# Kernel optimization log

Measured on AMD Instinct MI355X. Metric: run time of the kernel, lower is better.

The kernel has to match this reference:

```python
import jax, jax.numpy as jnp
import numpy as np

B, C, NQ, NK, S, H, FF = 8, 256, 1024, 4096, 16, 8, 2048
DH = C // H
EPS = 1e-5


def _layernorm(x, g, b):
    m = jnp.mean(x, axis=-1, keepdims=True)
    v = jnp.mean((x - m) ** 2, axis=-1, keepdims=True)
    return (x - m) * jax.lax.rsqrt(v + EPS) * g + b


def _box_query(key_pos, query_pos):
    # key_pos: (B,NK,3); query_pos: (B,NQ,6) = centers ++ box sizes (L,H,W)
    centers = query_pos[:, :, None, :3]            # (B,NQ,1,3)
    half = 0.5 * query_pos[:, :, None, 3:]         # (B,NQ,1,3)
    off = jnp.abs(key_pos[:, None, :, :] - centers)  # (B,NQ,NK,3)
    inside = jnp.all(off <= half, axis=-1)         # (B,NQ,NK)
    # first n_sample inside-points in index order (stable sort: inside first)
    order = jnp.argsort(~inside, axis=-1, stable=True)
    idx = order[..., :S]                           # (B,NQ,S)
    valid = jnp.take_along_axis(inside, idx, axis=-1)
    mask = ~valid                                  # True = padded / masked
    idx = jnp.where(mask, 0, idx)
    mask = mask.at[..., 0].set(False)              # matches cuda path: slot 0 never masked
    return idx, mask


def _forward(query, key, query_pos, key_pos,
             q_w, q_b, k_w, k_b, v_w, v_b, o_w, o_b,
             lin1_w, lin1_b, lin2_w, lin2_b,
             n1_g, n1_b, n2_g, n2_b, qpe_w, qpe_b, kpe_w, kpe_b):
    idx, mask = _box_query(key_pos, query_pos)     # (B,NQ,S), (B,NQ,S)
    # gather neighborhoods
    gxyz = jax.vmap(lambda kp, ix: kp[ix])(key_pos, idx)        # (B,NQ,S,3)
    gxyz = gxyz - query_pos[:, :, None, :3]                     # center-relative
    gfeat = jax.vmap(lambda kf, ix: kf[:, ix])(key, idx)        # (B,C,NQ,S)

    BQ = B * NQ
    kfeat = jnp.transpose(gfeat, (0, 2, 3, 1)).reshape(BQ, S, C)   # (BQ,S,C)
    kpe = gxyz.reshape(BQ, S, 3) @ kpe_w.T + kpe_b                 # cross_embed
    qtok = jnp.transpose(query, (0, 2, 1)).reshape(BQ, C)          # (BQ,C)
    qpe = (query_pos @ qpe_w.T + qpe_b).reshape(BQ, C)             # pos_embed

    # multihead cross-attention: 1 query vs S=16 local keys per group
    kv_in = kfeat + kpe
    qh = ((qtok + qpe) @ q_w.T + q_b).reshape(BQ, H, DH)
    kh = (kv_in @ k_w.T + k_b).reshape(BQ, S, H, DH)
    vh = (kv_in @ v_w.T + v_b).reshape(BQ, S, H, DH)
    scores = jnp.einsum('bhd,bshd->bhs', qh, kh) / np.sqrt(DH)    # (BQ,H,S)
    scores = jnp.where(mask.reshape(BQ, 1, S), -1e30, scores)
    attn = jax.nn.softmax(scores, axis=-1)
    ao = jnp.einsum('bhs,bshd->bhd', attn, vh).reshape(BQ, C)
    ao = ao @ o_w.T + o_b

    x = _layernorm(qtok + ao, n1_g, n1_b)                         # post-norm
    ff = jax.nn.relu(x @ lin1_w.T + lin1_b) @ lin2_w.T + lin2_b
    x = _layernorm(x + ff, n2_g, n2_b)
    return jnp.transpose(x.reshape(B, NQ, C), (0, 2, 1))          # (B,C,NQ)


def setup_inputs() -> dict:
    rng = jax.random.key(0)
    ks = jax.random.split(rng, 24)
    s = 0.02
    query = jax.random.normal(ks[0], (B, C, NQ), jnp.float32)
    key = jax.random.normal(ks[1], (B, C, NK), jnp.float32)
    key_pos = jax.random.uniform(ks[2], (B, NK, 3), jnp.float32)
    centers = jax.random.uniform(ks[3], (B, NQ, 3), jnp.float32)
    sizes = jax.random.uniform(ks[4], (B, NQ, 3), jnp.float32, minval=0.1, maxval=0.4)
    query_pos = jnp.concatenate([centers, sizes], axis=-1)
    p = {
        'q_w': jax.random.normal(ks[5], (C, C)) * s, 'q_b': jnp.zeros((C,)),
        'k_w': jax.random.normal(ks[6], (C, C)) * s, 'k_b': jnp.zeros((C,)),
        'v_w': jax.random.normal(ks[7], (C, C)) * s, 'v_b': jnp.zeros((C,)),
        'o_w': jax.random.normal(ks[8], (C, C)) * s, 'o_b': jnp.zeros((C,)),
        'lin1_w': jax.random.normal(ks[9], (FF, C)) * s, 'lin1_b': jnp.zeros((FF,)),
        'lin2_w': jax.random.normal(ks[10], (C, FF)) * s, 'lin2_b': jnp.zeros((C,)),
        'n1_g': jnp.ones((C,)), 'n1_b': jnp.zeros((C,)),
        'n2_g': jnp.ones((C,)), 'n2_b': jnp.zeros((C,)),
        'qpe_w': jax.random.normal(ks[11], (C, 6)) * s, 'qpe_b': jnp.zeros((C,)),
        'kpe_w': jax.random.normal(ks[12], (C, 3)) * s, 'kpe_b': jnp.zeros((C,)),
    }
    return dict(query=query, key=key, query_pos=query_pos, key_pos=key_pos, **p)


def reference(query, key, query_pos, key_pos,
              q_w, q_b, k_w, k_b, v_w, v_b, o_w, o_b,
              lin1_w, lin1_b, lin2_w, lin2_b,
              n1_g, n1_b, n2_g, n2_b, qpe_w, qpe_b, kpe_w, kpe_b):
    return _forward(query, key, query_pos, key_pos,
                    q_w, q_b, k_w, k_b, v_w, v_b, o_w, o_b,
                    lin1_w, lin1_b, lin2_w, lin2_b,
                    n1_g, n1_b, n2_g, n2_b, qpe_w, qpe_b, kpe_w, kpe_b)
```

## Files before the change

kernel.cpp:

```cpp
#include <hip/hip_runtime.h>
#include <cstdint>

#define B_   8
#define C_   256
#define NQ_  1024
#define NK_  4096
#define S_   16
#define H_   8
#define FF_  2048
#define DH_  32
#define BQ_  (B_*NQ_)
#define EPS_ 1e-5f

typedef __bf16 bf16x8 __attribute__((ext_vector_type(8)));
typedef __bf16 bf16x4 __attribute__((ext_vector_type(4)));
typedef float  f32x4  __attribute__((ext_vector_type(4)));

struct CvtArgs {
  const float* src[6];
  __bf16* dst[6];
};

__device__ __forceinline__ void gload_lds16(const void* g, void* l) {
  __builtin_amdgcn_global_load_lds(
      (const __attribute__((address_space(1))) void*)g,
      (__attribute__((address_space(3))) void*)l, 16, 0, 0);
}

#define SEGA 2048
#define SEGB 10240
#define SEGC 12288
#define SEGD 13568
#define NPREP 13584

__global__ __launch_bounds__(256) void k_prep(
    const float* __restrict__ query, const float* __restrict__ key,
    const float* __restrict__ query_pos, const float* __restrict__ key_pos,
    const float* __restrict__ qpe_w, const float* __restrict__ qpe_b,
    const float* __restrict__ k_w, const float* __restrict__ k_b,
    const float* __restrict__ v_w, const float* __restrict__ v_b,
    const float* __restrict__ kpe_w, const float* __restrict__ kpe_b,
    CvtArgs ca,
    __bf16* __restrict__ keyTb, __bf16* __restrict__ qtokb,
    __bf16* __restrict__ qinb,
    float4* __restrict__ Pk, float4* __restrict__ Pv,
    int* __restrict__ idxo, int* __restrict__ masko) {
  __shared__ __align__(16) float smem[1248];
  int blk = blockIdx.x, t = threadIdx.x;
  int tx = t & 31, ty = t >> 5;

  if (blk < SEGA) {
    int lane = t & 63;
    int q = blk * 4 + (t >> 6);
    int b = q >> 10;
    const float* kpb = key_pos + (size_t)b * NK_ * 3;
    const float* qp = query_pos + (size_t)q * 6;
    float cx = qp[0], cy = qp[1], cz = qp[2];
    float hx = 0.5f * qp[3], hy = 0.5f * qp[4], hz = 0.5f * qp[5];
    int* iq = idxo + (size_t)q * S_;
    int found = 0;
    for (int ch = 0; ch < NK_ / 64; ch += 4) {
      float dx[4], dy[4], dz[4];
#pragma unroll
      for (int u = 0; u < 4; ++u) {
        int k = (ch + u) * 64 + lane;
        dx[u] = fabsf(kpb[k * 3 + 0] - cx);
        dy[u] = fabsf(kpb[k * 3 + 1] - cy);
        dz[u] = fabsf(kpb[k * 3 + 2] - cz);
      }
#pragma unroll
      for (int u = 0; u < 4; ++u) {
        bool inside = (dx[u] <= hx) && (dy[u] <= hy) && (dz[u] <= hz);
        unsigned long long bal = __ballot(inside);
        if (inside) {
          int slot = found + __popcll(bal & ((1ull << lane) - 1ull));
          if (slot < S_) iq[slot] = (ch + u) * 64 + lane;
        }
        found += __popcll(bal);
      }
      if (found >= S_) break;
    }
    if (found > S_) found = S_;
    if (lane < S_) {
      int m = (lane < found) ? 0 : 1;
      if (lane >= found) iq[lane] = 0;
      if (lane == 0) m = 0;
      masko[(size_t)q * S_ + lane] = m;
    }
  } else if (blk < SEGB) {
    int local = blk - SEGA;
    float (*tt)[33] = (float(*)[33])smem;
    int x = local & 127, y = (local >> 7) & 7, z = local >> 10;
    int j0 = x * 32, i0 = y * 32;
    const float* inz = key + (size_t)z * C_ * NK_;
    __bf16* outz = keyTb + (size_t)z * NK_ * C_;
#pragma unroll
    for (int r = 0; r < 32; r += 8)
      tt[ty + r][tx] = inz[(size_t)(i0 + ty + r) * NK_ + (j0 + tx)];
    __syncthreads();
#pragma unroll
    for (int r = 0; r < 32; r += 8)
      outz[(size_t)(j0 + ty + r) * C_ + (i0 + tx)] = (__bf16)tt[tx][ty + r];
  } else if (blk < SEGC) {
    int local = blk - SEGB;
    float (*tt)[33] = (float(*)[33])smem;
    float (*sqp)[6] = (float(*)[6])(smem + 1056);
    int x = local & 31, y = (local >> 5) & 7, z = local >> 8;
    int nq0 = x * 32, c0 = y * 32;
    const float* inz = query + (size_t)z * C_ * NQ_;
#pragma unroll
    for (int r = 0; r < 32; r += 8)
      tt[ty + r][tx] = inz[(size_t)(c0 + ty + r) * NQ_ + (nq0 + tx)];
    if (t < 192)
      sqp[t / 6][t % 6] = query_pos[((size_t)z * NQ_ + nq0 + t / 6) * 6 + (t % 6)];
    int c = c0 + tx;
    float w0 = qpe_w[c * 6 + 0], w1 = qpe_w[c * 6 + 1], w2 = qpe_w[c * 6 + 2];
    float w3 = qpe_w[c * 6 + 3], w4 = qpe_w[c * 6 + 4], w5 = qpe_w[c * 6 + 5];
    float wb = qpe_b[c];
    __syncthreads();
#pragma unroll
    for (int r = 0; r < 32; r += 8) {
      int nql = ty + r;
      size_t row = (size_t)z * NQ_ + nq0 + nql;
      float v = tt[tx][nql];
      float pe = wb + sqp[nql][0] * w0 + sqp[nql][1] * w1 + sqp[nql][2] * w2 +
                 sqp[nql][3] * w3 + sqp[nql][4] * w4 + sqp[nql][5] * w5;
      qtokb[row * C_ + c] = (__bf16)v;
      qinb[row * C_ + c] = (__bf16)(v + pe);
    }
  } else if (blk < SEGD) {
    int local = blk - SEGC;
    int idx, base;
    if (local < 64)       { idx = 0; base = local; }
    else if (local < 128) { idx = 1; base = local - 64; }
    else if (local < 192) { idx = 2; base = local - 128; }
    else if (local < 256) { idx = 3; base = local - 192; }
    else if (local < 768) { idx = 4; base = local - 256; }
    else                  { idx = 5; base = local - 768; }
    size_t off = (size_t)base * 1024 + t * 4;
    float4 v = *(const float4*)(ca.src[idx] + off);
    __bf16* o = ca.dst[idx] + off;
    o[0] = (__bf16)v.x; o[1] = (__bf16)v.y; o[2] = (__bf16)v.z; o[3] = (__bf16)v.w;
  } else {
    int local = blk - SEGD;
    int bx = local & 7, bv = local >> 3;
    const float* w  = bv ? v_w : k_w;
    const float* wb = bv ? v_b : k_b;
    float4* P = bv ? Pv : Pk;
    float4 (*red)[8] = (float4(*)[8])smem;
    int nl = t >> 3, ks = (t & 7) * 32;
    int n = bx * 32 + nl;
    const float* wr = w + (size_t)n * C_;
    float p0 = 0.f, p1 = 0.f, p2 = 0.f, pb = 0.f;
#pragma unroll
    for (int k = ks; k < ks + 32; ++k) {
      float wv = wr[k];
      p0 += kpe_w[k * 3 + 0] * wv;
      p1 += kpe_w[k * 3 + 1] * wv;
      p2 += kpe_w[k * 3 + 2] * wv;
      pb += kpe_b[k] * wv;
    }
    red[nl][t & 7] = make_float4(p0, p1, p2, pb);
    __syncthreads();
    if (t < 32) {
      float4 s = red[t][0];
#pragma unroll
      for (int j = 1; j < 8; ++j) {
        float4 r = red[t][j];
        s.x += r.x; s.y += r.y; s.z += r.z; s.w += r.w;
      }
      s.w += wb[bx * 32 + t];
      P[bx * 32 + t] = s;
    }
  }
}

template <int BM, int BN>
__device__ __forceinline__ void gemm_tile(
    const __bf16* __restrict__ A, const __bf16* __restrict__ Wn,
    int m0, int n0, int K, int kbeg, int kend,
    __bf16 (*As)[64], __bf16 (*Bs)[64],
    f32x4 (&acc)[BM / 32][BN / 32]) {
  constexpr int MI = BM / 32, JN = BN / 32;
  constexpr int AI = BM / 32, BI = BN / 32;
  int t = threadIdx.x;
  int lane = t & 63, w = t >> 6;
  int lane16 = lane & 15, quad = lane >> 4;
  int wm = (w & 1) * (BM / 2), wn = (w >> 1) * (BN / 2);
  int l3 = lane >> 3;
  int lc = lane & 7;

  for (int k0 = kbeg; k0 < kend; k0 += 64) {
#pragma unroll
    for (int i = 0; i < AI; ++i) {
      int j = i * 4 + w;
      int row = j * 8 + l3;
      const __bf16* src = A + (size_t)(m0 + row) * K + k0 + ((lc ^ l3) << 3);
      gload_lds16(src, (char*)&As[0][0] + j * 1024);
    }
#pragma unroll
    for (int i = 0; i < BI; ++i) {
      int j = i * 4 + w;
      int row = j * 8 + l3;
      const __bf16* src = Wn + (size_t)(n0 + row) * K + k0 + ((lc ^ l3) << 3);
      gload_lds16(src, (char*)&Bs[0][0] + j * 1024);
    }
    __syncthreads();
#pragma unroll
    for (int kk = 0; kk < 64; kk += 32) {
      bf16x8 af[MI], bfr[JN];
      int qc = (kk >> 3) + quad;
#pragma unroll
      for (int i = 0; i < MI; ++i) {
        int row = wm + i * 16 + lane16;
        int ch = qc ^ (lane16 & 7);
        af[i] = *(const bf16x8*)((const char*)&As[row][0] + ch * 16);
      }
#pragma unroll
      for (int j = 0; j < JN; ++j) {
        int row = wn + j * 16 + lane16;
        int ch = qc ^ (lane16 & 7);
        bfr[j] = *(const bf16x8*)((const char*)&Bs[row][0] + ch * 16);
      }
#pragma unroll
      for (int i = 0; i < MI; ++i)
#pragma unroll
        for (int j = 0; j < JN; ++j)
          acc[i][j] = __builtin_amdgcn_mfma_f32_16x16x32_bf16(af[i], bfr[j], acc[i][j], 0, 0, 0);
    }
    __syncthreads();
  }
}

template <int BM, int BN, int RELU, int OUT_BF16>
__device__ __forceinline__ void gemm_body(
    const __bf16* __restrict__ A, const __bf16* __restrict__ Wn,
    const float* __restrict__ bias, void* __restrict__ outp,
    int n0, int m0, int N, int K, int kbeg, int kend) {
  constexpr int MI = BM / 32, JN = BN / 32;
  __shared__ __align__(16) __bf16 As[BM][64];
  __shared__ __align__(16) __bf16 Bs[BN][64];
  int t = threadIdx.x;
  int lane = t & 63, w = t >> 6;
  int lane16 = lane & 15, quad = lane >> 4;
  int wm = (w & 1) * (BM / 2), wn = (w >> 1) * (BN / 2);

  f32x4 acc[MI][JN];
#pragma unroll
  for (int i = 0; i < MI; ++i)
#pragma unroll
    for (int j = 0; j < JN; ++j) acc[i][j] = (f32x4){0.f, 0.f, 0.f, 0.f};

  gemm_tile<BM, BN>(A, Wn, m0, n0, K, kbeg, kend, As, Bs, acc);

#pragma unroll
  for (int j = 0; j < JN; ++j) {
    int col = n0 + wn + j * 16 + lane16;
    float bv = bias ? bias[col] : 0.f;
#pragma unroll
    for (int i = 0; i < MI; ++i) {
#pragma unroll
      for (int r = 0; r < 4; ++r) {
        int row = m0 + wm + i * 16 + quad * 4 + r;
        float v = acc[i][j][r] + bv;
        if (RELU) v = fmaxf(v, 0.f);
        if (OUT_BF16)
          ((__bf16*)outp)[(size_t)row * N + col] = (__bf16)v;
        else
          ((float*)outp)[(size_t)row * N + col] = v;
      }
    }
  }
}

template <int BM, int BN, int RELU, int OUT_BF16>
__global__ __launch_bounds__(256) void k_gemm(
    const __bf16* __restrict__ A, const __bf16* __restrict__ Wn,
    const float* __restrict__ bias, void* __restrict__ outp, int N, int K) {
  gemm_body<BM, BN, RELU, OUT_BF16>(A, Wn, bias, outp,
                                    blockIdx.x * BN, blockIdx.y * BM, N, K, 0, K);
}

__global__ __launch_bounds__(256) void k_gemm2(
    const __bf16* __restrict__ keyTb, const __bf16* __restrict__ kvwb,
    __bf16* __restrict__ khvbuf,
    const __bf16* __restrict__ qinb, const __bf16* __restrict__ qwb,
    const float* __restrict__ q_b, __bf16* __restrict__ qhb) {
  int blk = blockIdx.x;
  const __bf16 *A, *Wn; const float* bias; __bf16* outp; int n0, m0, N;
  if (blk < 1024) {
    A = keyTb; Wn = kvwb; bias = nullptr; outp = khvbuf;
    n0 = (blk & 3) * 128; m0 = (blk >> 2) * 128; N = 512;
  } else {
    int l = blk - 1024;
    A = qinb; Wn = qwb; bias = q_b; outp = qhb;
    n0 = (l & 1) * 128; m0 = (l >> 1) * 128; N = 256;
  }
  gemm_body<128, 128, 0, 1>(A, Wn, bias, outp, n0, m0, N, 256, 0, 256);
}

template <int K>
__device__ __forceinline__ void gemm32x256_sk2(
    const __bf16* __restrict__ A, const __bf16* __restrict__ Wn,
    const float* __restrict__ bias, int m0, char* smem, float (*buf)[257]) {
  constexpr int NT = K / 2 / 64;
  int t = threadIdx.x;
  int lane = t & 63, w = t >> 6;
  int kg = w >> 2, wl = w & 3;
  int lane16 = lane & 15, quad = lane >> 4;
  int wm = (wl & 1) * 16, wn = (wl >> 1) * 128;
  int l3 = lane >> 3, lc = lane & 7;
  int kbase = kg * (K / 2);

  char* As0 = smem + kg * 8192;
  char* Bs0 = smem + 16384 + kg * 65536;

  f32x4 acc[8];
#pragma unroll
  for (int j = 0; j < 8; ++j) acc[j] = (f32x4){0.f, 0.f, 0.f, 0.f};

  auto STAGE = [&](int bi, int ts) {
    int k0 = kbase + ts * 64;
    {
      int j = wl;
      int row = j * 8 + l3;
      const __bf16* src = A + (size_t)(m0 + row) * K + k0 + ((lc ^ l3) << 3);
      gload_lds16(src, As0 + bi * 4096 + j * 1024);
    }
#pragma unroll
    for (int i = 0; i < 8; ++i) {
      int j = i * 4 + wl;
      int row = j * 8 + l3;
      const __bf16* src = Wn + (size_t)row * K + k0 + ((lc ^ l3) << 3);
      gload_lds16(src, Bs0 + bi * 32768 + j * 1024);
    }
  };

  STAGE(0, 0);
  __syncthreads();
  int cur = 0;
  for (int ts = 0; ts < NT; ++ts) {
    if (ts + 1 < NT) STAGE(cur ^ 1, ts + 1);
    const char* Ab = As0 + cur * 4096;
    const char* Bb = Bs0 + cur * 32768;
#pragma unroll
    for (int kk = 0; kk < 64; kk += 32) {
      int qc = (kk >> 3) + quad;
      int ch = qc ^ (lane16 & 7);
      bf16x8 af = *(const bf16x8*)(Ab + (wm + lane16) * 128 + ch * 16);
      bf16x8 bfr[8];
#pragma unroll
      for (int j = 0; j < 8; ++j)
        bfr[j] = *(const bf16x8*)(Bb + (wn + j * 16 + lane16) * 128 + ch * 16);
#pragma unroll
      for (int j = 0; j < 8; ++j)
        acc[j] = __builtin_amdgcn_mfma_f32_16x16x32_bf16(af, bfr[j], acc[j], 0, 0, 0);
    }
    __syncthreads();
    cur ^= 1;
  }

  if (kg == 1) {
#pragma unroll
    for (int j = 0; j < 8; ++j) {
      int col = wn + j * 16 + lane16;
#pragma unroll
      for (int r = 0; r < 4; ++r)
        buf[wm + quad * 4 + r][col] = acc[j][r];
    }
  }
  __syncthreads();
  if (kg == 0) {
#pragma unroll
    for (int j = 0; j < 8; ++j) {
      int col = wn + j * 16 + lane16;
      float bv = bias[col];
#pragma unroll
      for (int r = 0; r < 4; ++r) {
        int row = wm + quad * 4 + r;
        buf[row][col] += acc[j][r] + bv;
      }
    }
  }
  __syncthreads();
}

__global__ __launch_bounds__(512) void k_oln(
    const __bf16* __restrict__ A , const __bf16* __restrict__ Wn ,
    const float* __restrict__ obias, const __bf16* __restrict__ qtokb,
    const float* __restrict__ g, const float* __restrict__ bb,
    __bf16* __restrict__ x1b) {
  __shared__ __align__(16) char smem[147456];
  float (*buf)[257] = (float(*)[257])smem;
  int m0 = blockIdx.x * 32;
  gemm32x256_sk2<C_>(A, Wn, obias, m0, smem, buf);

  int t = threadIdx.x;
  int lane = t & 63, w = t >> 6;
  float4 g4 = *(const float4*)(g + lane * 4);
  float4 b4 = *(const float4*)(bb + lane * 4);
#pragma unroll
  for (int rr = 0; rr < 4; ++rr) {
    int row = w * 4 + rr;
    size_t grow = (size_t)(m0 + row);
    bf16x4 q4 = *(const bf16x4*)&qtokb[grow * C_ + lane * 4];
    float x0 = buf[row][lane * 4 + 0] + (float)q4[0];
    float x1 = buf[row][lane * 4 + 1] + (float)q4[1];
    float x2 = buf[row][lane * 4 + 2] + (float)q4[2];
    float x3 = buf[row][lane * 4 + 3] + (float)q4[3];
    float s = x0 + x1 + x2 + x3;
#pragma unroll
    for (int off = 32; off >= 1; off >>= 1) s += __shfl_xor(s, off);
    float mean = s * (1.f / C_);
    float d0 = x0 - mean, d1 = x1 - mean, d2 = x2 - mean, d3 = x3 - mean;
    float v = d0 * d0 + d1 * d1 + d2 * d2 + d3 * d3;
#pragma unroll
    for (int off = 32; off >= 1; off >>= 1) v += __shfl_xor(v, off);
    float inv = 1.f / sqrtf(v * (1.f / C_) + EPS_);
    __bf16* obp = x1b + grow * C_ + lane * 4;
    obp[0] = (__bf16)(d0 * inv * g4.x + b4.x);
    obp[1] = (__bf16)(d1 * inv * g4.y + b4.y);
    obp[2] = (__bf16)(d2 * inv * g4.z + b4.z);
    obp[3] = (__bf16)(d3 * inv * g4.w + b4.w);
  }
}

__global__ __launch_bounds__(512) void k_ff2lnt(
    const __bf16* __restrict__ A , const __bf16* __restrict__ Wn ,
    const float* __restrict__ l2bias, const __bf16* __restrict__ x1b,
    const float* __restrict__ g, const float* __restrict__ bb,
    float* __restrict__ out) {
  __shared__ __align__(16) char smem[147456];
  float (*buf)[257] = (float(*)[257])smem;
  int m0 = blockIdx.x * 32;
  gemm32x256_sk2<FF_>(A, Wn, l2bias, m0, smem, buf);

  int t = threadIdx.x;
  int lane = t & 63, w = t >> 6;
  float4 g4 = *(const float4*)(g + lane * 4);
  float4 b4 = *(const float4*)(bb + lane * 4);
#pragma unroll
  for (int rr = 0; rr < 4; ++rr) {
    int row = w * 4 + rr;
    size_t grow = (size_t)(m0 + row);
    bf16x4 v4 = *(const bf16x4*)&x1b[grow * C_ + lane * 4];
    float x0 = buf[row][lane * 4 + 0] + (float)v4[0];
    float x1 = buf[row][lane * 4 + 1] + (float)v4[1];
    float x2 = buf[row][lane * 4 + 2] + (float)v4[2];
    float x3 = buf[row][lane * 4 + 3] + (float)v4[3];
    float s = x0 + x1 + x2 + x3;
#pragma unroll
    for (int off = 32; off >= 1; off >>= 1) s += __shfl_xor(s, off);
    float mean = s * (1.f / C_);
    float d0 = x0 - mean, d1 = x1 - mean, d2 = x2 - mean, d3 = x3 - mean;
    float v = d0 * d0 + d1 * d1 + d2 * d2 + d3 * d3;
#pragma unroll
    for (int off = 32; off >= 1; off >>= 1) v += __shfl_xor(v, off);
    float inv = 1.f / sqrtf(v * (1.f / C_) + EPS_);
    buf[row][lane * 4 + 0] = d0 * inv * g4.x + b4.x;
    buf[row][lane * 4 + 1] = d1 * inv * g4.y + b4.y;
    buf[row][lane * 4 + 2] = d2 * inv * g4.z + b4.z;
    buf[row][lane * 4 + 3] = d3 * inv * g4.w + b4.w;
  }
  __syncthreads();
  int z = m0 >> 10, nq0 = m0 & (NQ_ - 1);
  int tx = t & 31, ty = t >> 5;
#pragma unroll
  for (int ci = 0; ci < 16; ++ci) {
    int c = ci * 16 + ty;
    out[((size_t)z * C_ + c) * NQ_ + nq0 + tx] = buf[tx][c];
  }
}

__global__ __launch_bounds__(256) void k_attnf(
    const __bf16* __restrict__ khv,
    const float* __restrict__ key_pos,
    const float* __restrict__ query_pos,
    const int* __restrict__ idx,
    const int* __restrict__ maskb,
    const __bf16* __restrict__ qhb,
    const float4* __restrict__ Pk,
    const float4* __restrict__ Pv,
    __bf16* __restrict__ aob) {
  __shared__ __bf16 kvs[S_][520];
  __shared__ float qrow[C_];
  __shared__ float sc[H_][S_];
  __shared__ float pw[H_][S_];
  __shared__ float4 gx4[S_];
  __shared__ float4 pgxs[H_];
  __shared__ float4 qpks[H_];
  __shared__ int srow[S_], smask[S_];
  int bq = blockIdx.x, b = bq >> 10, t = threadIdx.x;

  if (t < S_) {
    int k = idx[(size_t)bq * S_ + t];
    srow[t] = b * NK_ + k;
    smask[t] = maskb[(size_t)bq * S_ + t];
    const float* kpp = key_pos + ((size_t)b * NK_ + k) * 3;
    const float* qp  = query_pos + (size_t)bq * 6;
    gx4[t] = make_float4(kpp[0] - qp[0], kpp[1] - qp[1], kpp[2] - qp[2], 1.f);
  }
  float qv_t = (float)qhb[(size_t)bq * C_ + t];
  qrow[t] = qv_t;
  {
    float4 p = Pk[t];
    p.x *= qv_t; p.y *= qv_t; p.z *= qv_t; p.w *= qv_t;
#pragma unroll
    for (int off = 16; off >= 1; off >>= 1) {
      p.x += __shfl_xor(p.x, off);
      p.y += __shfl_xor(p.y, off);
      p.z += __shfl_xor(p.z, off);
      p.w += __shfl_xor(p.w, off);
    }
    if ((t & 31) == 0) {
      const float s = 0.17677669529663687f;
      qpks[t >> 5] = make_float4(p.x * s, p.y * s, p.z * s, p.w * s);
    }
  }
  __syncthreads();
  {
    int s = t >> 4, c0 = (t & 15) * 32;
    const __bf16* src = khv + (size_t)srow[s] * 512 + c0;
    *(bf16x8*)&kvs[s][c0]      = *(const bf16x8*)&src[0];
    *(bf16x8*)&kvs[s][c0 + 8]  = *(const bf16x8*)&src[8];
    *(bf16x8*)&kvs[s][c0 + 16] = *(const bf16x8*)&src[16];
    *(bf16x8*)&kvs[s][c0 + 24] = *(const bf16x8*)&src[24];
  }
  __syncthreads();
  if (t < H_ * S_) {
    int h = t >> 4, s = t & (S_ - 1);
    float d = 0.f;
#pragma unroll
    for (int c0 = 0; c0 < 32; c0 += 8) {
      bf16x8 xv = *(const bf16x8*)&kvs[s][h * 32 + c0];
#pragma unroll
      for (int j = 0; j < 8; ++j) d += qrow[h * 32 + c0 + j] * (float)xv[j];
    }
    d *= 0.17677669529663687f;
    float4 g = gx4[s];
    float4 pk = qpks[h];
    d += g.x * pk.x + g.y * pk.y + g.z * pk.z + pk.w;
    if (smask[s]) d = -1e30f;
    sc[h][s] = d;
  }
  __syncthreads();
  if (t < H_) {
    float mx = -3.4e38f;
#pragma unroll
    for (int s = 0; s < S_; ++s) mx = fmaxf(mx, sc[t][s]);
    float e[S_], sum = 0.f;
#pragma unroll
    for (int s = 0; s < S_; ++s) { e[s] = expf(sc[t][s] - mx); sum += e[s]; }
    float inv = 1.f / sum;
    float gxx = 0.f, gyy = 0.f, gzz = 0.f;
#pragma unroll
    for (int s = 0; s < S_; ++s) {
      float p = e[s] * inv;
      pw[t][s] = p;
      float4 g = gx4[s];
      gxx += p * g.x; gyy += p * g.y; gzz += p * g.z;
    }
    pgxs[t] = make_float4(gxx, gyy, gzz, 1.f);
  }
  __syncthreads();
  {
    int h = t >> 5;
    float a = 0.f;
#pragma unroll
    for (int s = 0; s < S_; ++s) a += pw[h][s] * (float)kvs[s][256 + t];
    float4 pv = Pv[t];
    float4 g = pgxs[h];
    a += g.x * pv.x + g.y * pv.y + g.z * pv.z + pv.w;
    aob[(size_t)bq * C_ + t] = (__bf16)a;
  }
}

extern "C" void kernel_launch(void* const* d_in, const int* in_sizes, int n_in,
                              void* d_out, int out_size, void* d_ws, size_t ws_size,
                              hipStream_t stream) {
  const float* query     = (const float*)d_in[0];
  const float* key       = (const float*)d_in[1];
  const float* query_pos = (const float*)d_in[2];
  const float* key_pos   = (const float*)d_in[3];
  const float* q_w = (const float*)d_in[4];  const float* q_b = (const float*)d_in[5];
  const float* k_w = (const float*)d_in[6];  const float* k_b = (const float*)d_in[7];
  const float* v_w = (const float*)d_in[8];  const float* v_b = (const float*)d_in[9];
  const float* o_w = (const float*)d_in[10]; const float* o_b = (const float*)d_in[11];
  const float* lin1_w = (const float*)d_in[12]; const float* lin1_b = (const float*)d_in[13];
  const float* lin2_w = (const float*)d_in[14]; const float* lin2_b = (const float*)d_in[15];
  const float* n1_g = (const float*)d_in[16]; const float* n1_b = (const float*)d_in[17];
  const float* n2_g = (const float*)d_in[18]; const float* n2_b = (const float*)d_in[19];
  const float* qpe_w = (const float*)d_in[20]; const float* qpe_b = (const float*)d_in[21];
  const float* kpe_w = (const float*)d_in[22]; const float* kpe_b = (const float*)d_in[23];
  float* out = (float*)d_out;

  const size_t BQc = (size_t)BQ_ * C_;
  float* w = (float*)d_ws;
  size_t o = 0;
  __bf16* keyTb = (__bf16*)(w + o); o += (size_t)B_ * NK_ * C_ / 2;
  __bf16* qtokb = (__bf16*)(w + o); o += BQc / 2;
  __bf16* khvbuf = (__bf16*)(w + o); o += (size_t)B_ * NK_ * 512 / 2;
  __bf16* qinb = (__bf16*)(w + o); o += BQc / 2;
  __bf16* qhb  = (__bf16*)(w + o); o += BQc / 2;
  __bf16* aob  = (__bf16*)(w + o); o += BQc / 2;
  __bf16* x1b  = (__bf16*)(w + o); o += BQc / 2;
  __bf16* qwb  = (__bf16*)(w + o); o += (size_t)C_ * C_ / 2;
  __bf16* kvwb = (__bf16*)(w + o); o += (size_t)C_ * C_;
  __bf16* owb  = (__bf16*)(w + o); o += (size_t)C_ * C_ / 2;
  __bf16* l1b  = (__bf16*)(w + o); o += (size_t)C_ * FF_ / 2;
  __bf16* l2b  = (__bf16*)(w + o); o += (size_t)C_ * FF_ / 2;
  float4* Pk   = (float4*)(w + o); o += C_ * 4;
  float4* Pv   = (float4*)(w + o); o += C_ * 4;
  int* idxb  = (int*)(w + o); o += (size_t)BQ_ * S_;
  int* maskb = (int*)(w + o); o += (size_t)BQ_ * S_;
  __bf16* ff1b = khvbuf;

  CvtArgs ca;
  ca.src[0] = q_w; ca.dst[0] = qwb;
  ca.src[1] = k_w; ca.dst[1] = kvwb;
  ca.src[2] = v_w; ca.dst[2] = kvwb + (size_t)C_ * C_;
  ca.src[3] = o_w; ca.dst[3] = owb;
  ca.src[4] = lin1_w; ca.dst[4] = l1b;
  ca.src[5] = lin2_w; ca.dst[5] = l2b;
  k_prep<<<NPREP, 256, 0, stream>>>(query, key, query_pos, key_pos,
                                    qpe_w, qpe_b, k_w, k_b, v_w, v_b,
                                    kpe_w, kpe_b, ca,
                                    keyTb, qtokb, qinb, Pk, Pv, idxb, maskb);
  k_gemm2<<<1024 + 128, 256, 0, stream>>>(keyTb, kvwb, khvbuf, qinb, qwb, q_b, qhb);
  k_attnf<<<BQ_, 256, 0, stream>>>(khvbuf, key_pos, query_pos, idxb, maskb,
                                   qhb, Pk, Pv, aob);
  k_oln<<<BQ_ / 32, 512, 0, stream>>>(aob, owb, o_b, qtokb, n1_g, n1_b, x1b);
  k_gemm<128, 128, 1, 1><<<dim3(FF_ / 128, BQ_ / 128), 256, 0, stream>>>(
      x1b, l1b, lin1_b, ff1b, FF_, C_);
  k_ff2lnt<<<BQ_ / 32, 512, 0, stream>>>(ff1b, l2b, lin2_b, x1b, n2_g, n2_b, out);
}
```

Baseline: 246.7 us.

## Fuse FFN lin1 and lin2 into one kernel keeping hidden activations in LDS

Replaces the separate lin1 GEMM (writing a BQ×FF bf16 intermediate to global memory) and the lin2+LayerNorm kernel with one fused k_ffn kernel. Each 32-row block computes 256-wide chunks of the ReLU hidden activation into LDS and immediately multiplies them by the matching lin2 weight slice, streaming W1/W2 tiles through a 3-stage async LDS ring. This removes the 32 MB round trip of the FF intermediate and one launch. In exchange, each block re-reads all of W1 and W2 (L2 traffic), runs with only 256 blocks, and has a long serial dependency chain per block.

```diff
diff --git a/kernel.cpp b/kernel.cpp
--- a/kernel.cpp
+++ b/kernel.cpp
@@ -273,14 +273,6 @@
   }
 }
 
-template <int BM, int BN, int RELU, int OUT_BF16>
-__global__ __launch_bounds__(256) void k_gemm(
-    const __bf16* __restrict__ A, const __bf16* __restrict__ Wn,
-    const float* __restrict__ bias, void* __restrict__ outp, int N, int K) {
-  gemm_body<BM, BN, RELU, OUT_BF16>(A, Wn, bias, outp,
-                                    blockIdx.x * BN, blockIdx.y * BM, N, K, 0, K);
-}
-
 __global__ __launch_bounds__(256) void k_gemm2(
     const __bf16* __restrict__ keyTb, const __bf16* __restrict__ kvwb,
     __bf16* __restrict__ khvbuf,
@@ -425,18 +417,142 @@
   }
 }
 
-__global__ __launch_bounds__(512) void k_ff2lnt(
-    const __bf16* __restrict__ A , const __bf16* __restrict__ Wn ,
-    const float* __restrict__ l2bias, const __bf16* __restrict__ x1b,
+__global__ __launch_bounds__(512) void k_ffn(
+    const __bf16* __restrict__ x1b, const __bf16* __restrict__ W1,
+    const float* __restrict__ b1, const __bf16* __restrict__ W2,
+    const float* __restrict__ b2,
     const float* __restrict__ g, const float* __restrict__ bb,
     float* __restrict__ out) {
-  __shared__ __align__(16) char smem[147456];
+  __shared__ __align__(16) char smem[139264];
   float (*buf)[257] = (float(*)[257])smem;
+  char* Xs   = smem;
+  char* Ps   = smem + 16384;
+  char* ring = smem + 32768;
+  char* b1s  = smem + 131072;
   int m0 = blockIdx.x * 32;
-  gemm32x256_sk2<FF_>(A, Wn, l2bias, m0, smem, buf);
-
   int t = threadIdx.x;
   int lane = t & 63, w = t >> 6;
+  int lane16 = lane & 15, quad = lane >> 4;
+  int l3 = lane >> 3, lc = lane & 7;
+  int cw = w * 32;
+
+  f32x4 acc_out[2][2], acc_p[2][2];
+#pragma unroll
+  for (int i = 0; i < 2; ++i)
+#pragma unroll
+    for (int j = 0; j < 2; ++j) acc_out[i][j] = (f32x4){0.f, 0.f, 0.f, 0.f};
+
+#pragma unroll
+  for (int i = 0; i < 2; ++i) {
+    int j = i * 8 + w;
+    int row = j * 2 + (lane >> 5);
+    const __bf16* src = x1b + (size_t)(m0 + row) * C_ + (((lane & 31) ^ (row & 7)) << 3);
+    gload_lds16(src, Xs + j * 1024);
+  }
+  gload_lds16(b1 + w * 256 + lane * 4, b1s + w * 1024);
+
+  auto ISSUE = [&](int tau) {
+    int fc = tau >> 3, ph = (tau >> 2) & 1, ks = tau & 3;
+    char* dst = ring + (tau % 3) * 32768;
+#pragma unroll
+    for (int i = 0; i < 4; ++i) {
+      int j = i * 8 + w;
+      int row = j * 8 + l3;
+      const __bf16* src;
+      if (ph == 0)
+        src = W1 + (size_t)(fc * 256 + row) * C_ + ks * 64 + ((lc ^ l3) << 3);
+      else
+        src = W2 + (size_t)row * FF_ + fc * 256 + ks * 64 + ((lc ^ l3) << 3);
+      gload_lds16(src, dst + j * 1024);
+    }
+  };
+
+  ISSUE(0);
+  ISSUE(1);
+
+  for (int s = 0; s < 64; ++s) {
+    if (s < 62) {
+      ISSUE(s + 2);
+      asm volatile("s_waitcnt vmcnt(8)" ::: "memory");
+    } else if (s == 62) {
+      asm volatile("s_waitcnt vmcnt(4)" ::: "memory");
+    } else {
+      asm volatile("s_waitcnt vmcnt(0)" ::: "memory");
+    }
+    __builtin_amdgcn_s_barrier();
+    __builtin_amdgcn_sched_barrier(0);
+
+    int fc = s >> 3, ph = (s >> 2) & 1, ks = s & 3;
+    const char* Tb = ring + (s % 3) * 32768;
+    const char* Ab = ph ? Ps : Xs;
+    int qcb = ks * 8;
+
+    if (ph == 0 && ks == 0) {
+#pragma unroll
+      for (int i = 0; i < 2; ++i)
+#pragma unroll
+        for (int j = 0; j < 2; ++j) acc_p[i][j] = (f32x4){0.f, 0.f, 0.f, 0.f};
+    }
+
+#pragma unroll
+    for (int kk = 0; kk < 64; kk += 32) {
+      int q3 = (kk >> 3) + quad;
+      int swz3 = q3 ^ (lane16 & 7);
+      bf16x8 af[2], bfr[2];
+#pragma unroll
+      for (int rt = 0; rt < 2; ++rt)
+        af[rt] = *(const bf16x8*)(Ab + (rt * 16 + lane16) * 512 + (qcb + swz3) * 16);
+#pragma unroll
+      for (int ct = 0; ct < 2; ++ct)
+        bfr[ct] = *(const bf16x8*)(Tb + (cw + ct * 16 + lane16) * 128 + swz3 * 16);
+      if (ph == 0) {
+#pragma unroll
+        for (int rt = 0; rt < 2; ++rt)
+#pragma unroll
+          for (int ct = 0; ct < 2; ++ct)
+            acc_p[rt][ct] = __builtin_amdgcn_mfma_f32_16x16x32_bf16(af[rt], bfr[ct], acc_p[rt][ct], 0, 0, 0);
+      } else {
+#pragma unroll
+        for (int rt = 0; rt < 2; ++rt)
+#pragma unroll
+          for (int ct = 0; ct < 2; ++ct)
+            acc_out[rt][ct] = __builtin_amdgcn_mfma_f32_16x16x32_bf16(af[rt], bfr[ct], acc_out[rt][ct], 0, 0, 0);
+      }
+    }
+
+    if (ph == 0 && ks == 3) {
+#pragma unroll
+      for (int ct = 0; ct < 2; ++ct) {
+        int pcol = cw + ct * 16 + lane16;
+        float b1v = *(const float*)(b1s + (fc * 256 + pcol) * 4);
+#pragma unroll
+        for (int rt = 0; rt < 2; ++rt)
+#pragma unroll
+          for (int r = 0; r < 4; ++r) {
+            int prow = rt * 16 + quad * 4 + r;
+            float v = fmaxf(acc_p[rt][ct][r] + b1v, 0.f);
+            int chunk = pcol >> 3;
+            int byte = prow * 512 + ((chunk ^ (prow & 7)) << 4) + (pcol & 7) * 2;
+            *(__bf16*)(Ps + byte) = (__bf16)v;
+          }
+      }
+      asm volatile("s_waitcnt lgkmcnt(0)" ::: "memory");
+    }
+  }
+  __syncthreads();
+
+#pragma unroll
+  for (int ct = 0; ct < 2; ++ct) {
+    int col = cw + ct * 16 + lane16;
+    float b2v = b2[col];
+#pragma unroll
+    for (int rt = 0; rt < 2; ++rt)
+#pragma unroll
+      for (int r = 0; r < 4; ++r)
+        buf[rt * 16 + quad * 4 + r][col] = acc_out[rt][ct][r] + b2v;
+  }
+  __syncthreads();
+
   float4 g4 = *(const float4*)(g + lane * 4);
   float4 b4 = *(const float4*)(bb + lane * 4);
 #pragma unroll
@@ -463,6 +579,7 @@
     buf[row][lane * 4 + 3] = d3 * inv * g4.w + b4.w;
   }
   __syncthreads();
+
   int z = m0 >> 10, nq0 = m0 & (NQ_ - 1);
   int tx = t & 31, ty = t >> 5;
 #pragma unroll
@@ -613,7 +730,6 @@
   float4* Pv   = (float4*)(w + o); o += C_ * 4;
   int* idxb  = (int*)(w + o); o += (size_t)BQ_ * S_;
   int* maskb = (int*)(w + o); o += (size_t)BQ_ * S_;
-  __bf16* ff1b = khvbuf;
 
   CvtArgs ca;
   ca.src[0] = q_w; ca.dst[0] = qwb;
@@ -630,7 +746,6 @@
   k_attnf<<<BQ_, 256, 0, stream>>>(khvbuf, key_pos, query_pos, idxb, maskb,
                                    qhb, Pk, Pv, aob);
   k_oln<<<BQ_ / 32, 512, 0, stream>>>(aob, owb, o_b, qtokb, n1_g, n1_b, x1b);
-  k_gemm<128, 128, 1, 1><<<dim3(FF_ / 128, BQ_ / 128), 256, 0, stream>>>(
-      x1b, l1b, lin1_b, ff1b, FF_, C_);
-  k_ff2lnt<<<BQ_ / 32, 512, 0, stream>>>(ff1b, l2b, lin2_b, x1b, n2_g, n2_b, out);
-}
+  k_ffn<<<BQ_ / 32, 512, 0, stream>>>(x1b, l1b, lin1_b, l2b, lin2_b,
+                                      n2_g, n2_b, out);
+}
```

New measurement: 254.2 us. +3.0%, slower.

## Use full-width 64-row GEMM tiles for K/V projection and read K directly in attention

Applied to the files above, without the earlier changes.

The fused K/V and Q projection kernel now uses 64-row tiles spanning the full output width (512 or 256 columns), so each A tile is loaded once instead of being reloaded per 128-column block. This roughly halves the K/V block count and uses a large LDS B buffer with more accumulators per thread, which may cut occupancy. In the attention kernel only V rows are staged in shared memory, while K dot products read global memory directly. That removes a barrier and halves the LDS footprint, at the cost of uncoalesced global reads for K.

```diff
diff --git a/kernel.cpp b/kernel.cpp
--- a/kernel.cpp
+++ b/kernel.cpp
@@ -286,17 +286,55 @@
     __bf16* __restrict__ khvbuf,
     const __bf16* __restrict__ qinb, const __bf16* __restrict__ qwb,
     const float* __restrict__ q_b, __bf16* __restrict__ qhb) {
+  __shared__ __align__(16) __bf16 As[64][64];
+  __shared__ __align__(16) __bf16 Bs[512][64];
   int blk = blockIdx.x;
-  const __bf16 *A, *Wn; const float* bias; __bf16* outp; int n0, m0, N;
-  if (blk < 1024) {
-    A = keyTb; Wn = kvwb; bias = nullptr; outp = khvbuf;
-    n0 = (blk & 3) * 128; m0 = (blk >> 2) * 128; N = 512;
+  int t = threadIdx.x;
+  int lane = t & 63, w = t >> 6;
+  int lane16 = lane & 15, quad = lane >> 4;
+
+  if (blk < 512) {
+    int m0 = blk * 64;
+    int wm = (w & 1) * 32, wn = (w >> 1) * 256;
+    f32x4 acc[2][16];
+#pragma unroll
+    for (int i = 0; i < 2; ++i)
+#pragma unroll
+      for (int j = 0; j < 16; ++j) acc[i][j] = (f32x4){0.f, 0.f, 0.f, 0.f};
+    gemm_tile<64, 512>(keyTb, kvwb, m0, 0, 256, 0, 256, As, Bs, acc);
+#pragma unroll
+    for (int j = 0; j < 16; ++j) {
+      int col = wn + j * 16 + lane16;
+#pragma unroll
+      for (int i = 0; i < 2; ++i)
+#pragma unroll
+        for (int r = 0; r < 4; ++r) {
+          int row = m0 + wm + i * 16 + quad * 4 + r;
+          khvbuf[(size_t)row * 512 + col] = (__bf16)acc[i][j][r];
+        }
+    }
   } else {
-    int l = blk - 1024;
-    A = qinb; Wn = qwb; bias = q_b; outp = qhb;
-    n0 = (l & 1) * 128; m0 = (l >> 1) * 128; N = 256;
-  }
-  gemm_body<128, 128, 0, 1>(A, Wn, bias, outp, n0, m0, N, 256, 0, 256);
+    int m0 = (blk - 512) * 64;
+    int wm = (w & 1) * 32, wn = (w >> 1) * 128;
+    f32x4 acc[2][8];
+#pragma unroll
+    for (int i = 0; i < 2; ++i)
+#pragma unroll
+      for (int j = 0; j < 8; ++j) acc[i][j] = (f32x4){0.f, 0.f, 0.f, 0.f};
+    gemm_tile<64, 256>(qinb, qwb, m0, 0, 256, 0, 256, As, Bs, acc);
+#pragma unroll
+    for (int j = 0; j < 8; ++j) {
+      int col = wn + j * 16 + lane16;
+      float bv = q_b[col];
+#pragma unroll
+      for (int i = 0; i < 2; ++i)
+#pragma unroll
+        for (int r = 0; r < 4; ++r) {
+          int row = m0 + wm + i * 16 + quad * 4 + r;
+          qhb[(size_t)row * 256 + col] = (__bf16)(acc[i][j][r] + bv);
+        }
+    }
+  }
 }
 
 template <int K>
@@ -482,7 +520,7 @@
     const float4* __restrict__ Pk,
     const float4* __restrict__ Pv,
     __bf16* __restrict__ aob) {
-  __shared__ __bf16 kvs[S_][520];
+  __shared__ __bf16 vs[S_][264];
   __shared__ float qrow[C_];
   __shared__ float sc[H_][S_];
   __shared__ float pw[H_][S_];
@@ -519,20 +557,18 @@
   }
   __syncthreads();
   {
-    int s = t >> 4, c0 = (t & 15) * 32;
-    const __bf16* src = khv + (size_t)srow[s] * 512 + c0;
-    *(bf16x8*)&kvs[s][c0]      = *(const bf16x8*)&src[0];
-    *(bf16x8*)&kvs[s][c0 + 8]  = *(const bf16x8*)&src[8];
-    *(bf16x8*)&kvs[s][c0 + 16] = *(const bf16x8*)&src[16];
-    *(bf16x8*)&kvs[s][c0 + 24] = *(const bf16x8*)&src[24];
-  }
-  __syncthreads();
+    int s = t >> 4, c0 = (t & 15) * 16;
+    const __bf16* src = khv + (size_t)srow[s] * 512 + 256 + c0;
+    *(bf16x8*)&vs[s][c0]     = *(const bf16x8*)&src[0];
+    *(bf16x8*)&vs[s][c0 + 8] = *(const bf16x8*)&src[8];
+  }
   if (t < H_ * S_) {
     int h = t >> 4, s = t & (S_ - 1);
+    const __bf16* kp = khv + (size_t)srow[s] * 512 + h * 32;
     float d = 0.f;
 #pragma unroll
     for (int c0 = 0; c0 < 32; c0 += 8) {
-      bf16x8 xv = *(const bf16x8*)&kvs[s][h * 32 + c0];
+      bf16x8 xv = *(const bf16x8*)&kp[c0];
 #pragma unroll
       for (int j = 0; j < 8; ++j) d += qrow[h * 32 + c0 + j] * (float)xv[j];
     }
@@ -567,7 +603,7 @@
     int h = t >> 5;
     float a = 0.f;
 #pragma unroll
-    for (int s = 0; s < S_; ++s) a += pw[h][s] * (float)kvs[s][256 + t];
+    for (int s = 0; s < S_; ++s) a += pw[h][s] * (float)vs[s][t];
     float4 pv = Pv[t];
     float4 g = pgxs[h];
     a += g.x * pv.x + g.y * pv.y + g.z * pv.z + pv.w;
@@ -626,7 +662,7 @@
                                     qpe_w, qpe_b, k_w, k_b, v_w, v_b,
                                     kpe_w, kpe_b, ca,
                                     keyTb, qtokb, qinb, Pk, Pv, idxb, maskb);
-  k_gemm2<<<1024 + 128, 256, 0, stream>>>(keyTb, kvwb, khvbuf, qinb, qwb, q_b, qhb);
+  k_gemm2<<<512 + 128, 256, 0, stream>>>(keyTb, kvwb, khvbuf, qinb, qwb, q_b, qhb);
   k_attnf<<<BQ_, 256, 0, stream>>>(khvbuf, key_pos, query_pos, idxb, maskb,
                                    qhb, Pk, Pv, aob);
   k_oln<<<BQ_ / 32, 512, 0, stream>>>(aob, owb, o_b, qtokb, n1_g, n1_b, x1b);
```

New measurement: 253.2 us. +2.6%, slower.

## Replace split-K 32x256 GEMM with 8-warp N-split tiling and halved LDS

Applied to the files above, without the earlier changes.

The shared 32x256 GEMM used by the out-projection+LayerNorm and FF2+LayerNorm kernels drops its two-way split-K. All eight waves now cover the full K range, each owning a 32x32 output slice, and the split-K reduction pass through LDS is removed. Shared memory per block falls from 144KB to 72KB, which could let two blocks share a CU. The cost is a K loop twice as long per block and smaller per-wave tiles, so each wave re-reads the same A fragments.

```diff
diff --git a/kernel.cpp b/kernel.cpp
--- a/kernel.cpp
+++ b/kernel.cpp
@@ -300,39 +300,38 @@
 }
 
 template <int K>
-__device__ __forceinline__ void gemm32x256_sk2(
+__device__ __forceinline__ void gemm32x256_v3(
     const __bf16* __restrict__ A, const __bf16* __restrict__ Wn,
     const float* __restrict__ bias, int m0, char* smem, float (*buf)[257]) {
-  constexpr int NT = K / 2 / 64;
+  constexpr int NT = K / 64;
   int t = threadIdx.x;
   int lane = t & 63, w = t >> 6;
-  int kg = w >> 2, wl = w & 3;
   int lane16 = lane & 15, quad = lane >> 4;
-  int wm = (wl & 1) * 16, wn = (wl >> 1) * 128;
+  int wn = w * 32;
   int l3 = lane >> 3, lc = lane & 7;
-  int kbase = kg * (K / 2);
-
-  char* As0 = smem + kg * 8192;
-  char* Bs0 = smem + 16384 + kg * 65536;
-
-  f32x4 acc[8];
-#pragma unroll
-  for (int j = 0; j < 8; ++j) acc[j] = (f32x4){0.f, 0.f, 0.f, 0.f};
+
+  char* As0 = smem;
+  char* Bs0 = smem + 8192;
+
+  f32x4 acc[2][2];
+#pragma unroll
+  for (int i = 0; i < 2; ++i)
+#pragma unroll
+    for (int j = 0; j < 2; ++j) acc[i][j] = (f32x4){0.f, 0.f, 0.f, 0.f};
 
   auto STAGE = [&](int bi, int ts) {
-    int k0 = kbase + ts * 64;
-    {
-      int j = wl;
+    int k0 = ts * 64;
+    if (w < 4) {
+      int row = w * 8 + l3;
+      gload_lds16(A + (size_t)(m0 + row) * K + k0 + ((lc ^ l3) << 3),
+                  As0 + bi * 4096 + w * 1024);
+    }
+#pragma unroll
+    for (int i = 0; i < 4; ++i) {
+      int j = w * 4 + i;
       int row = j * 8 + l3;
-      const __bf16* src = A + (size_t)(m0 + row) * K + k0 + ((lc ^ l3) << 3);
-      gload_lds16(src, As0 + bi * 4096 + j * 1024);
-    }
-#pragma unroll
-    for (int i = 0; i < 8; ++i) {
-      int j = i * 4 + wl;
-      int row = j * 8 + l3;
-      const __bf16* src = Wn + (size_t)row * K + k0 + ((lc ^ l3) << 3);
-      gload_lds16(src, Bs0 + bi * 32768 + j * 1024);
+      gload_lds16(Wn + (size_t)row * K + k0 + ((lc ^ l3) << 3),
+                  Bs0 + bi * 32768 + j * 1024);
     }
   };
 
@@ -347,40 +346,32 @@
     for (int kk = 0; kk < 64; kk += 32) {
       int qc = (kk >> 3) + quad;
       int ch = qc ^ (lane16 & 7);
-      bf16x8 af = *(const bf16x8*)(Ab + (wm + lane16) * 128 + ch * 16);
-      bf16x8 bfr[8];
-#pragma unroll
-      for (int j = 0; j < 8; ++j)
+      bf16x8 af[2], bfr[2];
+#pragma unroll
+      for (int i = 0; i < 2; ++i)
+        af[i] = *(const bf16x8*)(Ab + (i * 16 + lane16) * 128 + ch * 16);
+#pragma unroll
+      for (int j = 0; j < 2; ++j)
         bfr[j] = *(const bf16x8*)(Bb + (wn + j * 16 + lane16) * 128 + ch * 16);
 #pragma unroll
-      for (int j = 0; j < 8; ++j)
-        acc[j] = __builtin_amdgcn_mfma_f32_16x16x32_bf16(af, bfr[j], acc[j], 0, 0, 0);
+      for (int i = 0; i < 2; ++i)
+#pragma unroll
+        for (int j = 0; j < 2; ++j)
+          acc[i][j] = __builtin_amdgcn_mfma_f32_16x16x32_bf16(af[i], bfr[j], acc[i][j], 0, 0, 0);
     }
     __syncthreads();
     cur ^= 1;
   }
 
-  if (kg == 1) {
-#pragma unroll
-    for (int j = 0; j < 8; ++j) {
-      int col = wn + j * 16 + lane16;
+#pragma unroll
+  for (int j = 0; j < 2; ++j) {
+    int col = wn + j * 16 + lane16;
+    float bv = bias[col];
+#pragma unroll
+    for (int i = 0; i < 2; ++i)
 #pragma unroll
       for (int r = 0; r < 4; ++r)
-        buf[wm + quad * 4 + r][col] = acc[j][r];
-    }
-  }
-  __syncthreads();
-  if (kg == 0) {
-#pragma unroll
-    for (int j = 0; j < 8; ++j) {
-      int col = wn + j * 16 + lane16;
-      float bv = bias[col];
-#pragma unroll
-      for (int r = 0; r < 4; ++r) {
-        int row = wm + quad * 4 + r;
-        buf[row][col] += acc[j][r] + bv;
-      }
-    }
+        buf[i * 16 + quad * 4 + r][col] = acc[i][j][r] + bv;
   }
   __syncthreads();
 }
@@ -390,10 +381,10 @@
     const float* __restrict__ obias, const __bf16* __restrict__ qtokb,
     const float* __restrict__ g, const float* __restrict__ bb,
     __bf16* __restrict__ x1b) {
-  __shared__ __align__(16) char smem[147456];
+  __shared__ __align__(16) char smem[73728];
   float (*buf)[257] = (float(*)[257])smem;
   int m0 = blockIdx.x * 32;
-  gemm32x256_sk2<C_>(A, Wn, obias, m0, smem, buf);
+  gemm32x256_v3<C_>(A, Wn, obias, m0, smem, buf);
 
   int t = threadIdx.x;
   int lane = t & 63, w = t >> 6;
@@ -430,10 +421,10 @@
     const float* __restrict__ l2bias, const __bf16* __restrict__ x1b,
     const float* __restrict__ g, const float* __restrict__ bb,
     float* __restrict__ out) {
-  __shared__ __align__(16) char smem[147456];
+  __shared__ __align__(16) char smem[73728];
   float (*buf)[257] = (float(*)[257])smem;
   int m0 = blockIdx.x * 32;
-  gemm32x256_sk2<FF_>(A, Wn, l2bias, m0, smem, buf);
+  gemm32x256_v3<FF_>(A, Wn, l2bias, m0, smem, buf);
 
   int t = threadIdx.x;
   int lane = t & 63, w = t >> 6;
```

Result: no change. 247.0 us (+0.1%).
